# Kernel tuning notes

Measured on AMD Instinct MI355X. Metric: run time of the kernel, lower is better.

Reference implementation:

```python
import jax, jax.numpy as jnp
import numpy as np

D = 256
H = 16
HD = D // H
N_BIAS = 6
B, E = 8, 1024


def _layernorm(x, g, b, eps=1e-5):
    mu = jnp.mean(x, axis=-1, keepdims=True)
    var = jnp.mean(jnp.square(x - mu), axis=-1, keepdims=True)
    return (x - mu) * jax.lax.rsqrt(var + eps) * g + b


def setup_inputs() -> dict:
    key = jax.random.key(0)
    ks = jax.random.split(key, 16)
    s = 0.02
    inp = {
        "x": jax.random.normal(ks[0], (B, E, D), dtype=jnp.float32),
        "struct_bias": jax.random.randint(ks[1], (B, E, E), 0, N_BIAS),
        "key_padding_mask": jnp.zeros((B, E), dtype=bool),
        # projections stored as [in, out] so y = x @ W + b
        "Wq": jax.random.normal(ks[2], (D, D), jnp.float32) * s,
        "bq": jnp.zeros((D,), jnp.float32),
        "Wk": jax.random.normal(ks[3], (D, D), jnp.float32) * s,
        "bk": jnp.zeros((D,), jnp.float32),
        "Wv": jax.random.normal(ks[4], (D, D), jnp.float32) * s,
        "bv": jnp.zeros((D,), jnp.float32),
        "Wo": jax.random.normal(ks[5], (D, D), jnp.float32) * s,
        "bo": jnp.zeros((D,), jnp.float32),
        "bias_emb": jax.random.normal(ks[6], (N_BIAS, H), jnp.float32) * s,
        "ln1_g": jnp.ones((D,), jnp.float32),
        "ln1_b": jnp.zeros((D,), jnp.float32),
        "W_ff1": jax.random.normal(ks[7], (D, 4 * D), jnp.float32) * s,
        "b_ff1": jnp.zeros((4 * D,), jnp.float32),
        "W_ff2": jax.random.normal(ks[8], (4 * D, D), jnp.float32) * s,
        "b_ff2": jnp.zeros((D,), jnp.float32),
        "ln2_g": jnp.ones((D,), jnp.float32),
        "ln2_b": jnp.zeros((D,), jnp.float32),
    }
    return inp


def reference(x, struct_bias, key_padding_mask, Wq, bq, Wk, bk, Wv, bv, Wo, bo,
              bias_emb, ln1_g, ln1_b, W_ff1, b_ff1, W_ff2, b_ff2, ln2_g, ln2_b):
    b, e, d = x.shape
    # project and split heads: [B, H, E, HD]
    q = (x @ Wq + bq).reshape(b, e, H, HD).transpose(0, 2, 1, 3)
    k = (x @ Wk + bk).reshape(b, e, H, HD).transpose(0, 2, 1, 3)
    v = (x @ Wv + bv).reshape(b, e, H, HD).transpose(0, 2, 1, 3)
    scores = jnp.einsum('bhqd,bhkd->bhqk', q, k) / np.sqrt(HD).astype(np.float32)
    # learned structural bias: [B,E,E,H] -> [B,H,E,E]
    bias = bias_emb[struct_bias].transpose(0, 3, 1, 2)
    scores = scores + bias
    scores = jnp.where(key_padding_mask[:, None, None, :], -jnp.inf, scores)
    attn = jax.nn.softmax(scores, axis=-1)
    out = jnp.einsum('bhqk,bhkd->bhqd', attn, v)
    out = out.transpose(0, 2, 1, 3).reshape(b, e, d)
    out = out @ Wo + bo
    x = _layernorm(x + out, ln1_g, ln1_b)
    ff = jax.nn.gelu(x @ W_ff1 + b_ff1, approximate=False) @ W_ff2 + b_ff2
    x = _layernorm(x + ff, ln2_g, ln2_b)
    return x
```

## Files before the change

kernel.cpp:

```cpp
#include <hip/hip_runtime.h>
#include <math.h>

#define B_  8
#define E_  1024
#define D_  256
#define H_  16
#define FF_ 1024
#define M_  (B_ * E_)

typedef __attribute__((ext_vector_type(8))) short short8;
typedef __attribute__((ext_vector_type(4))) float f32x4;
typedef unsigned short bf16u;

#define GLOAD_LDS16(g, l) __builtin_amdgcn_global_load_lds( \
    (const __attribute__((address_space(1))) void*)(g), \
    (__attribute__((address_space(3))) void*)(l), 16, 0, 0)

__device__ __forceinline__ unsigned short f2bf(float f) {
  union { float f; unsigned u; } c; c.f = f;
  unsigned r = c.u + 0x7fffu + ((c.u >> 16) & 1u);
  return (unsigned short)(r >> 16);
}
__device__ __forceinline__ float gelu_exact(float x) {
  return 0.5f * x * (1.0f + erff(x * 0.70710678118654752f));
}

template<int BM, int BN, int EPI>
__global__ __launch_bounds__(256) void mm_k(
    const bf16u* __restrict__ A, const bf16u* __restrict__ Wt,
    const float* __restrict__ bias, const float* __restrict__ R,
    void* __restrict__ Cout, int M, int N, int K)
{
  constexpr int WM = BM / 2, WN = BN / 2;
  constexpr int MT = WM / 16, NT = WN / 16;
  constexpr int PA = BM * 8 / 256, PB = BN * 8 / 256;
  constexpr int LBM = (BM == 128 ? 7 : 6), LBN = (BN == 128 ? 7 : 6);
  __shared__ bf16u As[BM * 64];
  __shared__ bf16u Bs[BN * 64];

  const int t = threadIdx.x;
  const int l15 = t & 15, quad = (t >> 4) & 3;
  const int w = t >> 6, wm = w >> 1, wn = w & 1;
  const int m0 = blockIdx.x * BM, n0 = blockIdx.y * BN;

  f32x4 acc[MT][NT];
  const f32x4 z4 = {0.f, 0.f, 0.f, 0.f};
#pragma unroll
  for (int i = 0; i < MT; ++i)
#pragma unroll
    for (int j = 0; j < NT; ++j) acc[i][j] = z4;

  for (int k0 = 0; k0 < K; k0 += 64) {
    __syncthreads();
#pragma unroll
    for (int p = 0; p < PA; ++p) {
      int g = p * 256 + t;
      int m = g & (BM - 1), c = g >> LBM;
      const bf16u* src = A + (size_t)(m0 + m) * K + k0 + c * 8;
      GLOAD_LDS16(src, As + g * 8);
    }
#pragma unroll
    for (int p = 0; p < PB; ++p) {
      int g = p * 256 + t;
      int n = g & (BN - 1), c = g >> LBN;
      const bf16u* src = Wt + (size_t)(n0 + n) * K + k0 + c * 8;
      GLOAD_LDS16(src, Bs + g * 8);
    }
    __syncthreads();
#pragma unroll
    for (int s = 0; s < 2; ++s) {
      short8 af[MT], bfr[NT];
#pragma unroll
      for (int mt = 0; mt < MT; ++mt)
        af[mt] = *(const short8*)(As + ((s * 4 + quad) * BM + wm * WM + mt * 16 + l15) * 8);
#pragma unroll
      for (int nt = 0; nt < NT; ++nt)
        bfr[nt] = *(const short8*)(Bs + ((s * 4 + quad) * BN + wn * WN + nt * 16 + l15) * 8);
#pragma unroll
      for (int mt = 0; mt < MT; ++mt)
#pragma unroll
        for (int nt = 0; nt < NT; ++nt)
          acc[mt][nt] = __builtin_amdgcn_mfma_f32_16x16x32_bf16(
              af[mt], bfr[nt], acc[mt][nt], 0, 0, 0);
    }
  }

#pragma unroll
  for (int mt = 0; mt < MT; ++mt) {
#pragma unroll
    for (int nt = 0; nt < NT; ++nt) {
      int col = n0 + wn * WN + nt * 16 + l15;
      float bia = bias[col];
#pragma unroll
      for (int r = 0; r < 4; ++r) {
        int row = m0 + wm * WM + mt * 16 + quad * 4 + r;
        size_t idx = (size_t)row * N + col;
        float v = acc[mt][nt][r] + bia;
        if (EPI == 2) { ((bf16u*)Cout)[idx] = f2bf(gelu_exact(v)); }
        else          { ((bf16u*)Cout)[idx] = f2bf(v); }
      }
    }
  }
}

template<int K_, int LN1>
__global__ __launch_bounds__(256) void mm_ln_k(
    const bf16u* __restrict__ A, const bf16u* __restrict__ Wt,
    const float* __restrict__ bias, const float* __restrict__ R,
    const float* __restrict__ gam, const float* __restrict__ bet,
    float* __restrict__ Yf, bf16u* __restrict__ Yb)
{
  __shared__ bf16u As[32 * 64];
  __shared__ bf16u Bs[256 * 64];
  __shared__ float red[2][32][4];

  const int t = threadIdx.x;
  const int l15 = t & 15, quad = (t >> 4) & 3;
  const int w = t >> 6;
  const int m0 = blockIdx.x * 32;

  f32x4 acc[2][4];
  const f32x4 z4 = {0.f, 0.f, 0.f, 0.f};
#pragma unroll
  for (int i = 0; i < 2; ++i)
#pragma unroll
    for (int j = 0; j < 4; ++j) acc[i][j] = z4;

  for (int k0 = 0; k0 < K_; k0 += 64) {
    __syncthreads();
    {
      const bf16u* src = A + (size_t)(m0 + (t & 31)) * K_ + k0 + (t >> 5) * 8;
      GLOAD_LDS16(src, As + t * 8);
    }
#pragma unroll
    for (int p = 0; p < 8; ++p) {
      int g = p * 256 + t;
      const bf16u* src = Wt + (size_t)(g & 255) * K_ + k0 + (g >> 8) * 8;
      GLOAD_LDS16(src, Bs + g * 8);
    }
    __syncthreads();
#pragma unroll
    for (int s = 0; s < 2; ++s) {
      const int cc = s * 4 + quad;
      short8 af[2], bfr[4];
#pragma unroll
      for (int mt = 0; mt < 2; ++mt)
        af[mt] = *(const short8*)(As + (cc * 32 + mt * 16 + l15) * 8);
#pragma unroll
      for (int nt = 0; nt < 4; ++nt)
        bfr[nt] = *(const short8*)(Bs + (cc * 256 + w * 64 + nt * 16 + l15) * 8);
#pragma unroll
      for (int mt = 0; mt < 2; ++mt)
#pragma unroll
        for (int nt = 0; nt < 4; ++nt)
          acc[mt][nt] = __builtin_amdgcn_mfma_f32_16x16x32_bf16(
              af[mt], bfr[nt], acc[mt][nt], 0, 0, 0);
    }
  }

  float ga[4], be4[4], bi[4];
#pragma unroll
  for (int nt = 0; nt < 4; ++nt) {
    int col = w * 64 + nt * 16 + l15;
    bi[nt] = bias[col]; ga[nt] = gam[col]; be4[nt] = bet[col];
  }
#pragma unroll
  for (int mt = 0; mt < 2; ++mt)
#pragma unroll
    for (int nt = 0; nt < 4; ++nt) {
      int col = w * 64 + nt * 16 + l15;
#pragma unroll
      for (int r = 0; r < 4; ++r) {
        int row = m0 + mt * 16 + quad * 4 + r;
        acc[mt][nt][r] += bi[nt] + R[(size_t)row * 256 + col];
      }
    }

  float s1[2][4], s2[2][4];
#pragma unroll
  for (int mt = 0; mt < 2; ++mt)
#pragma unroll
    for (int r = 0; r < 4; ++r) {
      float a = 0.f, b = 0.f;
#pragma unroll
      for (int nt = 0; nt < 4; ++nt) {
        float v = acc[mt][nt][r];
        a += v; b += v * v;
      }
      s1[mt][r] = a; s2[mt][r] = b;
    }
#pragma unroll
  for (int off = 1; off <= 8; off <<= 1)
#pragma unroll
    for (int mt = 0; mt < 2; ++mt)
#pragma unroll
      for (int r = 0; r < 4; ++r) {
        s1[mt][r] += __shfl_xor(s1[mt][r], off, 64);
        s2[mt][r] += __shfl_xor(s2[mt][r], off, 64);
      }
  if (l15 == 0) {
#pragma unroll
    for (int mt = 0; mt < 2; ++mt)
#pragma unroll
      for (int r = 0; r < 4; ++r) {
        int row32 = mt * 16 + quad * 4 + r;
        red[0][row32][w] = s1[mt][r];
        red[1][row32][w] = s2[mt][r];
      }
  }
  __syncthreads();

#pragma unroll
  for (int mt = 0; mt < 2; ++mt)
#pragma unroll
    for (int r = 0; r < 4; ++r) {
      int row32 = mt * 16 + quad * 4 + r;
      float4 sa = *(const float4*)&red[0][row32][0];
      float4 sb = *(const float4*)&red[1][row32][0];
      float sum = sa.x + sa.y + sa.z + sa.w;
      float sq  = sb.x + sb.y + sb.z + sb.w;
      float mu  = sum * (1.f / 256.f);
      float var = sq * (1.f / 256.f) - mu * mu;
      float rs  = 1.f / sqrtf(var + 1e-5f);
      int row = m0 + row32;
#pragma unroll
      for (int nt = 0; nt < 4; ++nt) {
        int col = w * 64 + nt * 16 + l15;
        float y = (acc[mt][nt][r] - mu) * rs * ga[nt] + be4[nt];
        size_t idx = (size_t)row * 256 + col;
        Yf[idx] = y;
        if (LN1) Yb[idx] = f2bf(y);
      }
    }
}

__global__ __launch_bounds__(256) void prep_k(
    const float* __restrict__ x, bf16u* __restrict__ xb,
    const float* __restrict__ Wq, const float* __restrict__ Wk,
    const float* __restrict__ Wv, const float* __restrict__ Wo,
    bf16u* __restrict__ Wqkvt, bf16u* __restrict__ Wot,
    const float* __restrict__ Wf1, bf16u* __restrict__ Wf1t,
    const float* __restrict__ Wf2, bf16u* __restrict__ Wf2t,
    const float* __restrict__ bq, const float* __restrict__ bk,
    const float* __restrict__ bv, float* __restrict__ bqkv)
{
  __shared__ float tile[32][33];
  const int bid = blockIdx.x;
  const int t = threadIdx.x;

  if (bid < 1024) {
    int i = bid * 256 + t;
    float4 a = ((const float4*)x)[i * 2];
    float4 b = ((const float4*)x)[i * 2 + 1];
    uint4 o;
    o.x = f2bf(a.x) | ((unsigned)f2bf(a.y) << 16);
    o.y = f2bf(a.z) | ((unsigned)f2bf(a.w) << 16);
    o.z = f2bf(b.x) | ((unsigned)f2bf(b.y) << 16);
    o.w = f2bf(b.z) | ((unsigned)f2bf(b.w) << 16);
    ((uint4*)xb)[i] = o;
  } else if (bid < 1792) {
    const float* src; bf16u* dst; int K, N, kb, nb;
    int rr = bid - 1024;
    if (rr < 256) {
      int z = rr >> 6, i = rr & 63;
      src = (z == 0) ? Wq : (z == 1) ? Wk : (z == 2) ? Wv : Wo;
      dst = (z == 0) ? Wqkvt : (z == 1) ? Wqkvt + 65536
          : (z == 2) ? Wqkvt + 131072 : Wot;
      K = 256; N = 256; kb = (i & 7) * 32; nb = (i >> 3) * 32;
    } else if (rr < 512) {
      int i = rr - 256;
      src = Wf1; dst = Wf1t; K = 256; N = 1024;
      kb = (i & 7) * 32; nb = (i >> 3) * 32;
    } else {
      int i = rr - 512;
      src = Wf2; dst = Wf2t; K = 1024; N = 256;
      kb = (i & 31) * 32; nb = (i >> 5) * 32;
    }
    const int tx = t & 31, ty = t >> 5;
#pragma unroll
    for (int r = 0; r < 4; ++r)
      tile[ty + 8 * r][tx] = src[(size_t)(kb + ty + 8 * r) * N + nb + tx];
    __syncthreads();
#pragma unroll
    for (int r = 0; r < 4; ++r)
      dst[(size_t)(nb + ty + 8 * r) * K + kb + tx] = f2bf(tile[tx][ty + 8 * r]);
  } else {
    for (int i = t; i < 768; i += 256)
      bqkv[i] = (i < 256) ? bq[i] : (i < 512) ? bk[i - 256] : bv[i - 512];
  }
}

__global__ __launch_bounds__(256) void attn_k(
    const bf16u* __restrict__ qkv, const int* __restrict__ sb,
    const unsigned char* __restrict__ mask, const float* __restrict__ be,
    bf16u* __restrict__ O)
{
  __shared__ bf16u Kl[2][64][40];
  __shared__ bf16u Vt[2][16][72];
  __shared__ bf16u Pl[4][16][40];
  __shared__ float embl[2][6];

  const int t    = threadIdx.x;
  const int b    = blockIdx.z;
  const int hg   = blockIdx.y;
  const int w    = t >> 6;
  const int lane = t & 63;
  const int l15  = lane & 15;
  const int quad = lane >> 4;
  const int q0w  = blockIdx.x * 64 + w * 16;

  if (t < 12) embl[t / 6][t % 6] = be[(t % 6) * 16 + hg * 2 + t / 6];

  {
    float4 z = {0.f, 0.f, 0.f, 0.f};
    float4* kp = (float4*)&Kl[0][0][0];
    for (int i = t; i < 640; i += 256) kp[i] = z;
  }

  short8 qf[2];
#pragma unroll
  for (int hp = 0; hp < 2; ++hp) {
    uint4 v = {0u, 0u, 0u, 0u};
    if (quad < 2)
      v = *(const uint4*)(qkv + ((size_t)(b * E_) + q0w + l15) * 768 +
                          (hg * 2 + hp) * 16 + quad * 8);
    else if (quad == 2)
      v.x = 0x3F80u;
    union { uint4 u; short8 s; } c; c.u = v;
    qf[hp] = c.s;
  }

  const int s_hp   = t >> 7;
  const int s_key  = (t >> 1) & 63;
  const int s_half = t & 1;
  const size_t kvbase = (size_t)b * E_ * 768;
  const int* sbp = sb + ((size_t)b * E_ + q0w) * E_;

  f32x4 accO[2];
  const f32x4 z4 = {0.f, 0.f, 0.f, 0.f};
  accO[0] = z4; accO[1] = z4;
  float lsum[2][4] = {};

  for (int k0 = 0; k0 < E_; k0 += 64) {
    int sbv[2][2][4];
#pragma unroll
    for (int s2 = 0; s2 < 2; ++s2)
#pragma unroll
      for (int f = 0; f < 2; ++f)
#pragma unroll
        for (int r = 0; r < 4; ++r)
          sbv[s2][f][r] = sbp[(size_t)(quad * 4 + r) * E_ + k0 + s2 * 32 + f * 16 + l15];

    __syncthreads();
    {
      const bf16u* kq = qkv + kvbase + (size_t)(k0 + s_key) * 768 + 256 +
                        (hg * 2 + s_hp) * 16 + s_half * 8;
      uint4 kw = *(const uint4*)kq;
      uint4 vw = *(const uint4*)(kq + 256);
      *(uint4*)&Kl[s_hp][s_key][s_half * 8] = kw;
      const int col = (s_key >> 5) * 32 + ((s_key & 15) << 1) + ((s_key >> 4) & 1);
      union { uint4 u; bf16u e[8]; } vc; vc.u = vw;
#pragma unroll
      for (int j = 0; j < 8; ++j)
        Vt[s_hp][s_half * 8 + j][col] = vc.e[j];
      if (s_half == 0) {
        unsigned char mv = mask[b * E_ + k0 + s_key];
        Kl[s_hp][s_key][16] = mv ? (bf16u)0xCF6E : (bf16u)0;
      }
    }
    __syncthreads();

#pragma unroll
    for (int hp = 0; hp < 2; ++hp) {
#pragma unroll
      for (int s2 = 0; s2 < 2; ++s2) {
        short8 kf0 = *(const short8*)&Kl[hp][s2 * 32 + l15][quad * 8];
        short8 kf1 = *(const short8*)&Kl[hp][s2 * 32 + 16 + l15][quad * 8];
        f32x4 sc0 = __builtin_amdgcn_mfma_f32_16x16x32_bf16(qf[hp], kf0, z4, 0, 0, 0);
        f32x4 sc1 = __builtin_amdgcn_mfma_f32_16x16x32_bf16(qf[hp], kf1, z4, 0, 0, 0);
#pragma unroll
        for (int r = 0; r < 4; ++r) {
          float w0 = embl[hp][sbv[s2][0][r]];
          float w1 = embl[hp][sbv[s2][1][r]];
          float p0 = __expf(fmaf(sc0[r], 0.25f, w0));
          float p1 = __expf(fmaf(sc1[r], 0.25f, w1));
          unsigned u0 = __float_as_uint(p0) & 0xffff0000u;
          unsigned u1 = __float_as_uint(p1) & 0xffff0000u;
          lsum[hp][r] += __uint_as_float(u0) + __uint_as_float(u1);
          *(unsigned*)&Pl[w][quad * 4 + r][l15 * 2] = (__float_as_uint(p0) >> 16) | u1;
        }
        short8 pf = *(const short8*)&Pl[w][l15][quad * 8];
        short8 vf = *(const short8*)&Vt[hp][l15][s2 * 32 + quad * 8];
        accO[hp] = __builtin_amdgcn_mfma_f32_16x16x32_bf16(pf, vf, accO[hp], 0, 0, 0);
      }
    }
  }

#pragma unroll
  for (int off = 1; off <= 8; off <<= 1)
#pragma unroll
    for (int hp = 0; hp < 2; ++hp)
#pragma unroll
      for (int r = 0; r < 4; ++r)
        lsum[hp][r] += __shfl_xor(lsum[hp][r], off, 64);

#pragma unroll
  for (int hp = 0; hp < 2; ++hp) {
#pragma unroll
    for (int r = 0; r < 4; ++r) {
      float o = accO[hp][r] / lsum[hp][r];
      O[((size_t)(b * E_) + q0w + quad * 4 + r) * 256 + (hg * 2 + hp) * 16 + l15] = f2bf(o);
    }
  }
}

extern "C" void kernel_launch(void* const* d_in, const int* in_sizes, int n_in,
                              void* d_out, int out_size, void* d_ws, size_t ws_size,
                              hipStream_t stream) {
  const float* x   = (const float*)d_in[0];
  const int*   sb  = (const int*)d_in[1];
  const unsigned char* mask = (const unsigned char*)d_in[2];
  const float* Wq  = (const float*)d_in[3];
  const float* bq  = (const float*)d_in[4];
  const float* Wk  = (const float*)d_in[5];
  const float* bk  = (const float*)d_in[6];
  const float* Wv  = (const float*)d_in[7];
  const float* bv  = (const float*)d_in[8];
  const float* Wo  = (const float*)d_in[9];
  const float* bo  = (const float*)d_in[10];
  const float* be  = (const float*)d_in[11];
  const float* g1  = (const float*)d_in[12];
  const float* b1  = (const float*)d_in[13];
  const float* Wf1 = (const float*)d_in[14];
  const float* bf1 = (const float*)d_in[15];
  const float* Wf2 = (const float*)d_in[16];
  const float* bf2 = (const float*)d_in[17];
  const float* g2  = (const float*)d_in[18];
  const float* b2  = (const float*)d_in[19];
  float* out = (float*)d_out;

  char* ws = (char*)d_ws;
  bf16u* Wqkvt = (bf16u*)(ws + 0);
  bf16u* Wot   = (bf16u*)(ws + 393216);
  bf16u* Wf1t  = (bf16u*)(ws + 524288);
  bf16u* Wf2t  = (bf16u*)(ws + 1048576);
  float* bqkv  = (float*)(ws + 1572864);
  bf16u* xb    = (bf16u*)(ws + 2097152);
  bf16u* qkv   = (bf16u*)(ws + 6291456);
  bf16u* att   = (bf16u*)(ws + 18874368);
  float* x1    = (float*)(ws + 23068672);
  bf16u* x1b   = (bf16u*)(ws + 31457280);
  bf16u* ffh   = (bf16u*)(ws + 2097152);

  dim3 blk(256);

  prep_k<<<1793, blk, 0, stream>>>(x, xb, Wq, Wk, Wv, Wo, Wqkvt, Wot,
                                   Wf1, Wf1t, Wf2, Wf2t, bq, bk, bv, bqkv);

  mm_k<128, 128, 0><<<dim3(64, 6), blk, 0, stream>>>(xb, Wqkvt, bqkv, nullptr,
                                                     qkv, M_, 768, 256);
  attn_k<<<dim3(16, 8, 8), blk, 0, stream>>>(qkv, sb, mask, be, att);

  mm_ln_k<256, 1><<<256, blk, 0, stream>>>(att, Wot, bo, x, g1, b1, x1, x1b);

  mm_k<128, 128, 2><<<dim3(64, 8), blk, 0, stream>>>(x1b, Wf1t, bf1, nullptr,
                                                     ffh, M_, 1024, 256);
  mm_ln_k<1024, 0><<<256, blk, 0, stream>>>(ffh, Wf2t, bf2, x1, g2, b2, out, nullptr);
}
```

Measured before the change: 243.9 us.

## Double-buffer LDS tiles in GEMM kernels and shrink projection tile to 128x64

Adds double-buffered shared-memory staging to the projection GEMMs and the GEMM+LayerNorm kernels. The next K tile's async global-to-LDS loads are issued before computing on the current one, with explicit vmcnt/lgkmcnt waits plus barriers instead of two __syncthreads per iteration. This aims to hide global load latency. The QKV and FF1 GEMMs also move from 128x128 to 128x64 tiles, doubling the grid for better CU occupancy. The cost is doubled LDS use, with 64KB+ per block in mm_ln_p, which may reduce occupancy. The hand-counted vmcnt values are fragile.

```diff
diff --git a/kernel.cpp b/kernel.cpp
--- a/kernel.cpp
+++ b/kernel.cpp
@@ -16,6 +16,9 @@
     (const __attribute__((address_space(1))) void*)(g), \
     (__attribute__((address_space(3))) void*)(l), 16, 0, 0)
 
+#define LGKM_BAR()  asm volatile("s_waitcnt lgkmcnt(0)\ns_barrier" ::: "memory")
+#define VM_BAR(N)   asm volatile("s_waitcnt vmcnt(" #N ")\ns_barrier" ::: "memory")
+
 __device__ __forceinline__ unsigned short f2bf(float f) {
   union { float f; unsigned u; } c; c.f = f;
   unsigned r = c.u + 0x7fffu + ((c.u >> 16) & 1u);
@@ -25,24 +28,37 @@
   return 0.5f * x * (1.0f + erff(x * 0.70710678118654752f));
 }
 
-template<int BM, int BN, int EPI>
-__global__ __launch_bounds__(256) void mm_k(
+template<int K_, int EPI>
+__global__ __launch_bounds__(256) void mm_p(
     const bf16u* __restrict__ A, const bf16u* __restrict__ Wt,
-    const float* __restrict__ bias, const float* __restrict__ R,
-    void* __restrict__ Cout, int M, int N, int K)
+    const float* __restrict__ bias, void* __restrict__ Cout, int N)
 {
-  constexpr int WM = BM / 2, WN = BN / 2;
-  constexpr int MT = WM / 16, NT = WN / 16;
-  constexpr int PA = BM * 8 / 256, PB = BN * 8 / 256;
-  constexpr int LBM = (BM == 128 ? 7 : 6), LBN = (BN == 128 ? 7 : 6);
-  __shared__ bf16u As[BM * 64];
-  __shared__ bf16u Bs[BN * 64];
+  constexpr int BM = 128, BN = 64, KT = K_ / 64;
+  constexpr int MT = 4, NT = 2;
+  __shared__ bf16u As[2][BM * 64];
+  __shared__ bf16u Bs[2][BN * 64];
 
   const int t = threadIdx.x;
   const int l15 = t & 15, quad = (t >> 4) & 3;
   const int w = t >> 6, wm = w >> 1, wn = w & 1;
   const int m0 = blockIdx.x * BM, n0 = blockIdx.y * BN;
 
+  auto stage = [&](int kt, int pb) {
+    const int k0 = kt * 64;
+#pragma unroll
+    for (int p = 0; p < 4; ++p) {
+      int g = p * 256 + t;
+      int m = g & 127, c = g >> 7;
+      GLOAD_LDS16(A + (size_t)(m0 + m) * K_ + k0 + c * 8, &As[pb][g * 8]);
+    }
+#pragma unroll
+    for (int p = 0; p < 2; ++p) {
+      int g = p * 256 + t;
+      int n = g & 63, c = g >> 6;
+      GLOAD_LDS16(Wt + (size_t)(n0 + n) * K_ + k0 + c * 8, &Bs[pb][g * 8]);
+    }
+  };
+
   f32x4 acc[MT][NT];
   const f32x4 z4 = {0.f, 0.f, 0.f, 0.f};
 #pragma unroll
@@ -50,32 +66,24 @@
 #pragma unroll
     for (int j = 0; j < NT; ++j) acc[i][j] = z4;
 
-  for (int k0 = 0; k0 < K; k0 += 64) {
-    __syncthreads();
-#pragma unroll
-    for (int p = 0; p < PA; ++p) {
-      int g = p * 256 + t;
-      int m = g & (BM - 1), c = g >> LBM;
-      const bf16u* src = A + (size_t)(m0 + m) * K + k0 + c * 8;
-      GLOAD_LDS16(src, As + g * 8);
-    }
-#pragma unroll
-    for (int p = 0; p < PB; ++p) {
-      int g = p * 256 + t;
-      int n = g & (BN - 1), c = g >> LBN;
-      const bf16u* src = Wt + (size_t)(n0 + n) * K + k0 + c * 8;
-      GLOAD_LDS16(src, Bs + g * 8);
-    }
-    __syncthreads();
+  stage(0, 0);
+#pragma unroll
+  for (int kt = 0; kt < KT; ++kt) {
+    LGKM_BAR();
+    if (kt + 1 < KT) { stage(kt + 1, (kt + 1) & 1); VM_BAR(6); }
+    else             { VM_BAR(0); }
+    const bf16u* Ab = As[kt & 1];
+    const bf16u* Bb = Bs[kt & 1];
 #pragma unroll
     for (int s = 0; s < 2; ++s) {
+      const int cc = s * 4 + quad;
       short8 af[MT], bfr[NT];
 #pragma unroll
       for (int mt = 0; mt < MT; ++mt)
-        af[mt] = *(const short8*)(As + ((s * 4 + quad) * BM + wm * WM + mt * 16 + l15) * 8);
+        af[mt] = *(const short8*)(Ab + (cc * BM + wm * 64 + mt * 16 + l15) * 8);
 #pragma unroll
       for (int nt = 0; nt < NT; ++nt)
-        bfr[nt] = *(const short8*)(Bs + ((s * 4 + quad) * BN + wn * WN + nt * 16 + l15) * 8);
+        bfr[nt] = *(const short8*)(Bb + (cc * BN + wn * 32 + nt * 16 + l15) * 8);
 #pragma unroll
       for (int mt = 0; mt < MT; ++mt)
 #pragma unroll
@@ -89,29 +97,30 @@
   for (int mt = 0; mt < MT; ++mt) {
 #pragma unroll
     for (int nt = 0; nt < NT; ++nt) {
-      int col = n0 + wn * WN + nt * 16 + l15;
+      int col = n0 + wn * 32 + nt * 16 + l15;
       float bia = bias[col];
 #pragma unroll
       for (int r = 0; r < 4; ++r) {
-        int row = m0 + wm * WM + mt * 16 + quad * 4 + r;
+        int row = m0 + wm * 64 + mt * 16 + quad * 4 + r;
         size_t idx = (size_t)row * N + col;
         float v = acc[mt][nt][r] + bia;
-        if (EPI == 2) { ((bf16u*)Cout)[idx] = f2bf(gelu_exact(v)); }
-        else          { ((bf16u*)Cout)[idx] = f2bf(v); }
+        if (EPI == 2) ((bf16u*)Cout)[idx] = f2bf(gelu_exact(v));
+        else          ((bf16u*)Cout)[idx] = f2bf(v);
       }
     }
   }
 }
 
 template<int K_, int LN1>
-__global__ __launch_bounds__(256) void mm_ln_k(
+__global__ __launch_bounds__(256) void mm_ln_p(
     const bf16u* __restrict__ A, const bf16u* __restrict__ Wt,
     const float* __restrict__ bias, const float* __restrict__ R,
     const float* __restrict__ gam, const float* __restrict__ bet,
     float* __restrict__ Yf, bf16u* __restrict__ Yb)
 {
-  __shared__ bf16u As[32 * 64];
-  __shared__ bf16u Bs[256 * 64];
+  constexpr int KT = K_ / 64;
+  __shared__ bf16u As[2][32 * 64];
+  __shared__ bf16u Bs[2][256 * 64];
   __shared__ float red[2][32][4];
 
   const int t = threadIdx.x;
@@ -119,6 +128,18 @@
   const int w = t >> 6;
   const int m0 = blockIdx.x * 32;
 
+  auto stage = [&](int kt, int pb) {
+    const int k0 = kt * 64;
+    GLOAD_LDS16(A + (size_t)(m0 + (t & 31)) * K_ + k0 + (t >> 5) * 8,
+                &As[pb][t * 8]);
+#pragma unroll
+    for (int p = 0; p < 8; ++p) {
+      int g = p * 256 + t;
+      GLOAD_LDS16(Wt + (size_t)(g & 255) * K_ + k0 + (g >> 8) * 8,
+                  &Bs[pb][g * 8]);
+    }
+  };
+
   f32x4 acc[2][4];
   const f32x4 z4 = {0.f, 0.f, 0.f, 0.f};
 #pragma unroll
@@ -126,29 +147,24 @@
 #pragma unroll
     for (int j = 0; j < 4; ++j) acc[i][j] = z4;
 
-  for (int k0 = 0; k0 < K_; k0 += 64) {
-    __syncthreads();
-    {
-      const bf16u* src = A + (size_t)(m0 + (t & 31)) * K_ + k0 + (t >> 5) * 8;
-      GLOAD_LDS16(src, As + t * 8);
-    }
-#pragma unroll
-    for (int p = 0; p < 8; ++p) {
-      int g = p * 256 + t;
-      const bf16u* src = Wt + (size_t)(g & 255) * K_ + k0 + (g >> 8) * 8;
-      GLOAD_LDS16(src, Bs + g * 8);
-    }
-    __syncthreads();
+  stage(0, 0);
+#pragma unroll
+  for (int kt = 0; kt < KT; ++kt) {
+    LGKM_BAR();
+    if (kt + 1 < KT) { stage(kt + 1, (kt + 1) & 1); VM_BAR(9); }
+    else             { VM_BAR(0); }
+    const bf16u* Ab = As[kt & 1];
+    const bf16u* Bb = Bs[kt & 1];
 #pragma unroll
     for (int s = 0; s < 2; ++s) {
       const int cc = s * 4 + quad;
       short8 af[2], bfr[4];
 #pragma unroll
       for (int mt = 0; mt < 2; ++mt)
-        af[mt] = *(const short8*)(As + (cc * 32 + mt * 16 + l15) * 8);
+        af[mt] = *(const short8*)(Ab + (cc * 32 + mt * 16 + l15) * 8);
 #pragma unroll
       for (int nt = 0; nt < 4; ++nt)
-        bfr[nt] = *(const short8*)(Bs + (cc * 256 + w * 64 + nt * 16 + l15) * 8);
+        bfr[nt] = *(const short8*)(Bb + (cc * 256 + w * 64 + nt * 16 + l15) * 8);
 #pragma unroll
       for (int mt = 0; mt < 2; ++mt)
 #pragma unroll
@@ -208,7 +224,7 @@
         red[1][row32][w] = s2[mt][r];
       }
   }
-  __syncthreads();
+  LGKM_BAR();
 
 #pragma unroll
   for (int mt = 0; mt < 2; ++mt)
@@ -457,13 +473,13 @@
   prep_k<<<1793, blk, 0, stream>>>(x, xb, Wq, Wk, Wv, Wo, Wqkvt, Wot,
                                    Wf1, Wf1t, Wf2, Wf2t, bq, bk, bv, bqkv);
 
-  mm_k<128, 128, 0><<<dim3(64, 6), blk, 0, stream>>>(xb, Wqkvt, bqkv, nullptr,
-                                                     qkv, M_, 768, 256);
+  mm_p<256, 0><<<dim3(64, 12), blk, 0, stream>>>(xb, Wqkvt, bqkv, qkv, 768);
+
   attn_k<<<dim3(16, 8, 8), blk, 0, stream>>>(qkv, sb, mask, be, att);
 
-  mm_ln_k<256, 1><<<256, blk, 0, stream>>>(att, Wot, bo, x, g1, b1, x1, x1b);
-
-  mm_k<128, 128, 2><<<dim3(64, 8), blk, 0, stream>>>(x1b, Wf1t, bf1, nullptr,
-                                                     ffh, M_, 1024, 256);
-  mm_ln_k<1024, 0><<<256, blk, 0, stream>>>(ffh, Wf2t, bf2, x1, g2, b2, out, nullptr);
-}
+  mm_ln_p<256, 1><<<256, blk, 0, stream>>>(att, Wot, bo, x, g1, b1, x1, x1b);
+
+  mm_p<256, 2><<<dim3(64, 16), blk, 0, stream>>>(x1b, Wf1t, bf1, ffh, 1024);
+
+  mm_ln_p<1024, 0><<<256, blk, 0, stream>>>(ffh, Wf2t, bf2, x1, g2, b2, out, nullptr);
+}
```

New measurement: 244.9 us. Within noise of the previous version (+0.4%).
